# Kernel optimization log

Measured on AMD Instinct MI355X. Metric: run time of the kernel, lower is better.

## Reference

```python
import jax, jax.numpy as jnp
import numpy as np

D_MODEL = 1024
N_HEADS = 16
HEAD_DIM = D_MODEL // N_HEADS


def setup_inputs() -> dict:
    key = jax.random.key(0)
    ks = jax.random.split(key, 9)
    s = 0.02
    x = jax.random.normal(ks[0], (2, 2048, D_MODEL), dtype=jnp.float32)
    wq = jax.random.normal(ks[1], (D_MODEL, D_MODEL), dtype=jnp.float32) * s
    wk = jax.random.normal(ks[2], (D_MODEL, D_MODEL), dtype=jnp.float32) * s
    wv = jax.random.normal(ks[3], (D_MODEL, D_MODEL), dtype=jnp.float32) * s
    wo = jax.random.normal(ks[4], (D_MODEL, D_MODEL), dtype=jnp.float32) * s
    bq = jax.random.normal(ks[5], (D_MODEL,), dtype=jnp.float32) * s
    bk = jax.random.normal(ks[6], (D_MODEL,), dtype=jnp.float32) * s
    bv = jax.random.normal(ks[7], (D_MODEL,), dtype=jnp.float32) * s
    bo = jax.random.normal(ks[8], (D_MODEL,), dtype=jnp.float32) * s
    return {"x": x, "wq": wq, "bq": bq, "wk": wk, "bk": bk,
            "wv": wv, "bv": bv, "wo": wo, "bo": bo}


def reference(x, wq, bq, wk, bk, wv, bv, wo, bo):
    B, T, C = x.shape
    H, Dh = N_HEADS, HEAD_DIM
    # torch Linear: y = x @ W.T + b
    q = (x @ wq.T + bq).reshape(B, T, H, Dh).transpose(0, 2, 1, 3)  # [B,H,T,Dh]
    k = (x @ wk.T + bk).reshape(B, T, H, Dh).transpose(0, 2, 1, 3)
    v = (x @ wv.T + bv).reshape(B, T, H, Dh).transpose(0, 2, 1, 3)
    scale = 1.0 / jnp.sqrt(jnp.float32(Dh))
    score = jnp.einsum('bhqd,bhkd->bhqk', q, k) * scale  # [B,H,T,T]
    causal = jnp.triu(jnp.ones((T, T), dtype=jnp.bool_), k=1)
    score = jnp.where(causal[None, None], jnp.float32(-10000.0), score)
    attn = jax.nn.softmax(score, axis=-1)
    out = jnp.einsum('bhqk,bhkd->bhqd', attn, v)  # [B,H,T,Dh]
    out = out.transpose(0, 2, 1, 3).reshape(B, T, C)
    return out @ wo.T + bo
```

## Files before the change

kernel.cpp:

```cpp
#include <hip/hip_runtime.h>
#include <hip/hip_bf16.h>

typedef __bf16 bf16_t;
typedef __bf16 bf16x8 __attribute__((ext_vector_type(8)));
typedef __bf16 bf16x4 __attribute__((ext_vector_type(4)));
typedef float f32x4 __attribute__((ext_vector_type(4)));
typedef unsigned int u32;

#define D_MODEL 1024
#define T_SEQ   2048
#define N_HEADS 16

#define WAITVM(N) asm volatile("s_waitcnt vmcnt(" #N ")" ::: "memory")

__device__ __forceinline__ void gload_lds16(const void* g, void* l) {
  __builtin_amdgcn_global_load_lds((const __attribute__((address_space(1))) u32*)g,
                                   (__attribute__((address_space(3))) u32*)l, 16, 0, 0);
}

__device__ __forceinline__ float fast_exp2(float x) {
#if __has_builtin(__builtin_amdgcn_exp2f)
  return __builtin_amdgcn_exp2f(x);
#else
  return __expf(x * 0.69314718056f);
#endif
}

struct CastArgs { const float* src[5]; bf16_t* dst[5]; };

__global__ __launch_bounds__(256) void cast_all(CastArgs p) {
  unsigned i = (blockIdx.x * 256u + threadIdx.x) * 4u;
  int seg; unsigned off;
  if (i < 4194304u) { seg = 0; off = i; }
  else { unsigned r = i - 4194304u; seg = 1 + (int)(r >> 20); off = r & 1048575u; }
  const float4 v = *(const float4*)(p.src[seg] + off);
  bf16x4 o = { (bf16_t)v.x, (bf16_t)v.y, (bf16_t)v.z, (bf16_t)v.w };
  *(bf16x4*)(p.dst[seg] + off) = o;
}

#define QSCL 0.18033688011112042f

struct QKVArgs {
  const bf16_t* A;
  const bf16_t* W[3];
  const float* bias[3];
  bf16_t* out[3];
};

__global__ __launch_bounds__(512, 2) void qkv_gemm(QKVArgs p) {
  __shared__ bf16_t lds[2 * 28672];

  const int tid = threadIdx.x;
  const int l = tid & 63, wid = tid >> 6;
  const int lh = l >> 4, r15 = l & 15;

  const int lid = blockIdx.x;
  const int bx = lid >> 4, by = lid & 15;
  const int brow = bx * 256;
  const int gcol0 = by * 192;

  const int wr = (wid >> 2) * 128;
  const int wc = (wid & 3) * 48;
  const int wrc = (wr >> 4);
  const int wcc = (wc >> 4);
  const int sA = (lh ^ ((r15 >> 1) & 3)) * 8;
  const int roff = r15 * 32;

  const int srow = l >> 2;
  const int gs = ((l & 3) ^ ((l >> 3) & 3)) * 8;

  f32x4 acc[8][3];
  const f32x4 zero = {0.f, 0.f, 0.f, 0.f};
#pragma unroll
  for (int i = 0; i < 8; ++i)
#pragma unroll
    for (int j = 0; j < 3; ++j) acc[i][j] = zero;

  const bf16_t* A = p.A;

  auto stageA = [&](bf16_t* buf, int k0, int kh) {
#pragma unroll
    for (int i = 0; i < 2; ++i) {
      int c = wid * 2 + i;
      gload_lds16(A + (size_t)(brow + c * 16 + srow) * D_MODEL + k0 + kh * 32 + gs,
                  buf + kh * 8192 + c * 512);
    }
  };
  auto stageB = [&](bf16_t* buf, int k0) {
#pragma unroll
    for (int i = 0; i < 3; ++i) {
      int g = wid * 3 + i;
      int kh = g >= 12;
      int c = g - kh * 12;
      int gcol = gcol0 + c * 16 + srow;
      int z = gcol >> 10;
      const bf16_t* w = (z == 0) ? p.W[0] : ((z == 1) ? p.W[1] : p.W[2]);
      gload_lds16(w + (size_t)(gcol & 1023) * D_MODEL + k0 + kh * 32 + gs,
                  buf + 16384 + kh * 6144 + c * 512);
    }
  };

  stageA(lds, 0, 0);
  stageA(lds, 0, 1);
  stageB(lds, 0);
  WAITVM(0);
  __builtin_amdgcn_s_barrier();

  for (int t = 0; t < 16; ++t) {
    bf16_t* cur = lds + (t & 1) * 28672;
    bf16_t* nxt = lds + ((t + 1) & 1) * 28672;
    const int k1 = (t + 1) * 64;
    const bool more = (t < 15);

    bf16x8 bfr[3][2];
#pragma unroll
    for (int ph = 0; ph < 4; ++ph) {
      bf16x8 a[2][2];
#pragma unroll
      for (int jj = 0; jj < 2; ++jj)
#pragma unroll
        for (int kh = 0; kh < 2; ++kh)
          a[jj][kh] = *(const bf16x8*)(cur + kh * 8192 + (wrc + 2 * ph + jj) * 512 + roff + sA);
      if (ph == 0) {
#pragma unroll
        for (int ni = 0; ni < 3; ++ni)
#pragma unroll
          for (int kh = 0; kh < 2; ++kh)
            bfr[ni][kh] = *(const bf16x8*)(cur + 16384 + kh * 6144 + (wcc + ni) * 512 + roff + sA);
      }
      if (more) {
        if (ph == 0) stageA(nxt, k1, 0);
        else if (ph == 1) stageA(nxt, k1, 1);
        else if (ph == 2) stageB(nxt, k1);
      }
      __builtin_amdgcn_s_barrier();
      __builtin_amdgcn_s_setprio(1);
#pragma unroll
      for (int jj = 0; jj < 2; ++jj)
#pragma unroll
        for (int ni = 0; ni < 3; ++ni) {
          acc[2 * ph + jj][ni] = __builtin_amdgcn_mfma_f32_16x16x32_bf16(a[jj][0], bfr[ni][0], acc[2 * ph + jj][ni], 0, 0, 0);
          acc[2 * ph + jj][ni] = __builtin_amdgcn_mfma_f32_16x16x32_bf16(a[jj][1], bfr[ni][1], acc[2 * ph + jj][ni], 0, 0, 0);
        }
      __builtin_amdgcn_s_setprio(0);
      if (ph == 3 && more) WAITVM(0);
      __builtin_amdgcn_s_barrier();
    }
  }

#pragma unroll
  for (int ni = 0; ni < 3; ++ni) {
    const int col = gcol0 + wc + ni * 16 + r15;
    const int z = col >> 10;
    const int zc = col & 1023;
    const float* bias = (z == 0) ? p.bias[0] : ((z == 1) ? p.bias[1] : p.bias[2]);
    bf16_t* O = (z == 0) ? p.out[0] : ((z == 1) ? p.out[1] : p.out[2]);
    const float bz = bias[zc];
    if (z == 2) {
#pragma unroll
      for (int mi = 0; mi < 8; ++mi) {
        int row0 = brow + wr + mi * 16 + lh * 4;
        int bb = row0 >> 11, t0 = row0 & 2047;
        bf16x4 pk;
#pragma unroll
        for (int j = 0; j < 4; ++j) pk[j] = (bf16_t)(acc[mi][ni][j] + bz);
        *(bf16x4*)(O + (size_t)bb * (D_MODEL * T_SEQ) + (size_t)zc * T_SEQ + t0) = pk;
      }
    } else if (z == 0) {
#pragma unroll
      for (int mi = 0; mi < 8; ++mi) {
        int row0 = brow + wr + mi * 16 + lh * 4;
#pragma unroll
        for (int j = 0; j < 4; ++j)
          O[(size_t)(row0 + j) * D_MODEL + zc] = (bf16_t)((acc[mi][ni][j] + bz) * QSCL);
      }
    } else {
#pragma unroll
      for (int mi = 0; mi < 8; ++mi) {
        int row0 = brow + wr + mi * 16 + lh * 4;
#pragma unroll
        for (int j = 0; j < 4; ++j)
          O[(size_t)(row0 + j) * D_MODEL + zc] = (bf16_t)(acc[mi][ni][j] + bz);
      }
    }
  }
}

__device__ __forceinline__ void stage_ab64(
    const bf16_t* __restrict__ A, const bf16_t* __restrict__ W,
    bf16_t* buf, int brow, int bcol, int k0, int w, int l) {
  const int srow = l >> 2;
  const int scol = ((l & 3) ^ ((l >> 3) & 3)) * 8;
#pragma unroll
  for (int i = 0; i < 3; ++i) {
    int ch = w * 3 + i;
    const bf16_t* src = (ch < 4)
      ? A + (size_t)(brow + ch * 16 + srow) * D_MODEL + k0 + scol
      : W + (size_t)(bcol + (ch - 4) * 16 + srow) * D_MODEL + k0 + scol;
    gload_lds16(src, buf + ch * 512);
  }
}

__device__ __forceinline__ void gemm_tile_64(
    const bf16_t* __restrict__ A, const bf16_t* __restrict__ W,
    bf16_t* bufs, int brow, int bcol, f32x4 acc[2][4])
{
  const int tid = threadIdx.x;
  const int l = tid & 63, w = tid >> 6;
  const int wr = (w >> 1) * 32, wc = (w & 1) * 64;
  const int lh = l >> 4, r15 = l & 15;
  const int NS = D_MODEL / 32;

  stage_ab64(A, W, bufs + 0 * 6144, brow, bcol, 0, w, l);
  stage_ab64(A, W, bufs + 1 * 6144, brow, bcol, 32, w, l);

  for (int t = 0; t < NS; ++t) {
    bf16_t* bb = bufs + (t % 3) * 6144;
    if (t + 2 < NS) {
      stage_ab64(A, W, bufs + ((t + 2) % 3) * 6144, brow, bcol, (t + 2) * 32, w, l);
      WAITVM(6);
    } else if (t + 1 < NS) {
      WAITVM(3);
    } else {
      WAITVM(0);
    }
    __builtin_amdgcn_s_barrier();

    bf16x8 af[2], bfr[4];
#pragma unroll
    for (int mi = 0; mi < 2; ++mi) {
      int rr = wr + mi * 16 + r15;
      int s = lh ^ ((rr >> 1) & 3);
      af[mi] = *(const bf16x8*)(bb + rr * 32 + s * 8);
    }
#pragma unroll
    for (int ni = 0; ni < 4; ++ni) {
      int rr = wc + ni * 16 + r15;
      int s = lh ^ ((rr >> 1) & 3);
      bfr[ni] = *(const bf16x8*)(bb + 2048 + rr * 32 + s * 8);
    }
    __builtin_amdgcn_s_setprio(1);
#pragma unroll
    for (int mi = 0; mi < 2; ++mi)
#pragma unroll
      for (int ni = 0; ni < 4; ++ni)
        acc[mi][ni] = __builtin_amdgcn_mfma_f32_16x16x32_bf16(af[mi], bfr[ni], acc[mi][ni], 0, 0, 0);
    __builtin_amdgcn_s_setprio(0);
    __builtin_amdgcn_s_barrier();
  }
}

__global__ __launch_bounds__(256) void out_gemm(
    const bf16_t* __restrict__ A, const bf16_t* __restrict__ W,
    const float* __restrict__ bias, float* __restrict__ O)
{
  __shared__ bf16_t bufs[3 * 6144];
  f32x4 acc[2][4];
  f32x4 zero = {0.f, 0.f, 0.f, 0.f};
#pragma unroll
  for (int i = 0; i < 2; ++i)
#pragma unroll
    for (int j = 0; j < 4; ++j) acc[i][j] = zero;

  const int brow = blockIdx.x * 64, bcol = blockIdx.y * 128;
  gemm_tile_64(A, W, bufs, brow, bcol, acc);

  const int tid = threadIdx.x, l = tid & 63, w = tid >> 6;
  const int wr = (w >> 1) * 32, wc = (w & 1) * 64, lh = l >> 4, r15 = l & 15;
#pragma unroll
  for (int ni = 0; ni < 4; ++ni) {
    int col = bcol + wc + ni * 16 + r15;
    float bz = bias[col];
#pragma unroll
    for (int mi = 0; mi < 2; ++mi) {
      int row0 = brow + wr + mi * 16 + lh * 4;
#pragma unroll
      for (int j = 0; j < 4; ++j)
        O[(size_t)(row0 + j) * D_MODEL + col] = acc[mi][ni][j] + bz;
    }
  }
}

__device__ __forceinline__ void stage_kv(const bf16_t* Kg, const bf16_t* Vg,
                                         bf16_t* Kd, bf16_t* Vd, int kv0, int w, int l) {
#pragma unroll
  for (int i = 0; i < 2; ++i) {
    int c = w * 2 + i;
    int rr = c * 8 + (l >> 3);
    int gcol = ((l & 7) ^ ((l >> 3) & 7)) * 8;
    gload_lds16(Kg + (size_t)(kv0 + rr) * D_MODEL + gcol, Kd + c * 512);
    gload_lds16(Vg + (size_t)rr * T_SEQ + kv0 + gcol, Vd + c * 512);
  }
}

__global__ __launch_bounds__(256) void flash_attn(
    const bf16_t* __restrict__ Qm, const bf16_t* __restrict__ Km,
    const bf16_t* __restrict__ Vtg, bf16_t* __restrict__ Om)
{
  __shared__ bf16_t Kls[2][64 * 64];
  __shared__ bf16_t Vls[2][64 * 64];
  __shared__ bf16_t Pls[4][16 * 64];

  const int tid = threadIdx.x, l = tid & 63, w = tid >> 6;
  const int lh = l >> 4, r15 = l & 15;

  const int lid = blockIdx.x;
  const int xcd = lid & 7;
  const int idx = lid >> 3;
  const int pair = idx & 15;
  const int bh = xcd + 8 * (idx >> 4);
  const int b = bh >> 4, h = bh & 15;
  const int qtA = pair, qtB = 31 - pair;

  const size_t baseQ = (size_t)b * T_SEQ * D_MODEL + h * 64;
  const size_t baseVt = (size_t)b * (D_MODEL * T_SEQ) + (size_t)(h * 64) * T_SEQ;
  const bf16_t* Kg = Km + baseQ;
  const bf16_t* Vg = Vtg + baseVt;

  int qw = qtA * 64 + w * 16;

  bf16x8 qf[2];
  {
    const bf16_t* qp = Qm + baseQ + (size_t)(qw + r15) * D_MODEL + lh * 8;
    qf[0] = *(const bf16x8*)(qp);
    qf[1] = *(const bf16x8*)(qp + 32);
  }

  float l_r = 0.f;
  f32x4 o_acc[4];
  const f32x4 zero = {0.f, 0.f, 0.f, 0.f};
#pragma unroll
  for (int n = 0; n < 4; ++n) o_acc[n] = zero;

  bf16_t* P = &Pls[w][0];
  const int NT = 33;

  stage_kv(Kg, Vg, Kls[0], Vls[0], 0, w, l);

  for (int t = 0; t < NT; ++t) {
    const int buf = t & 1;
    if (t + 1 < NT) {
      const int nt = t + 1;
      const int nkv0 = (nt <= qtA) ? nt * 64 : (nt - qtA - 1) * 64;
      stage_kv(Kg, Vg, Kls[buf ^ 1], Vls[buf ^ 1], nkv0, w, l);
      WAITVM(4);
    } else {
      WAITVM(0);
    }
    __builtin_amdgcn_s_barrier();

    const int kv0 = (t <= qtA) ? t * 64 : (t - qtA - 1) * 64;
    const bool diag = (t == qtA) || (t == NT - 1);
    const bf16_t* Kb = Kls[buf];
    const bf16_t* Vb = Vls[buf];

    f32x4 sf[4];
    __builtin_amdgcn_s_setprio(1);
#pragma unroll
    for (int n = 0; n < 4; ++n) {
      const int kvc = n * 16 + r15;
      const int sw = kvc & 7;
      bf16x8 kf0 = *(const bf16x8*)(Kb + kvc * 64 + ((lh ^ sw) * 8));
      bf16x8 kf1 = *(const bf16x8*)(Kb + kvc * 64 + (((4 + lh) ^ sw) * 8));
      f32x4 a = zero;
      a = __builtin_amdgcn_mfma_f32_16x16x32_bf16(kf0, qf[0], a, 0, 0, 0);
      a = __builtin_amdgcn_mfma_f32_16x16x32_bf16(kf1, qf[1], a, 0, 0, 0);
      sf[n] = a;
    }
    __builtin_amdgcn_s_setprio(0);

    const int qrow = qw + r15;
#pragma unroll
    for (int n = 0; n < 4; ++n) {
      float pv[4];
      if (diag) {
#pragma unroll
        for (int j = 0; j < 4; ++j) {
          const int kvcol = kv0 + n * 16 + lh * 4 + j;
          float pp = fast_exp2(sf[n][j]);
          if (kvcol > qrow) pp = 0.f;
          pv[j] = pp;
          l_r += pp;
        }
      } else {
#pragma unroll
        for (int j = 0; j < 4; ++j) {
          float pp = fast_exp2(sf[n][j]);
          pv[j] = pp;
          l_r += pp;
        }
      }
      bf16x4 pk = { (bf16_t)pv[0], (bf16_t)pv[1], (bf16_t)pv[2], (bf16_t)pv[3] };
      const int slot = n * 2 + (lh >> 1);
      *(bf16x4*)(P + r15 * 64 + ((slot ^ (r15 & 7)) * 8) + (lh & 1) * 4) = pk;
    }

    bf16x8 pa0, pa1;
    {
      const int sw = r15 & 7;
      pa0 = *(const bf16x8*)(P + r15 * 64 + ((lh ^ sw) * 8));
      pa1 = *(const bf16x8*)(P + r15 * 64 + (((4 + lh) ^ sw) * 8));
    }
    __builtin_amdgcn_s_setprio(1);
#pragma unroll
    for (int n = 0; n < 4; ++n) {
      const int d = n * 16 + r15;
      const int sw = d & 7;
      bf16x8 vf0 = *(const bf16x8*)(Vb + d * 64 + ((lh ^ sw) * 8));
      bf16x8 vf1 = *(const bf16x8*)(Vb + d * 64 + (((4 + lh) ^ sw) * 8));
      o_acc[n] = __builtin_amdgcn_mfma_f32_16x16x32_bf16(vf0, pa0, o_acc[n], 0, 0, 0);
      o_acc[n] = __builtin_amdgcn_mfma_f32_16x16x32_bf16(vf1, pa1, o_acc[n], 0, 0, 0);
    }
    __builtin_amdgcn_s_setprio(0);

    __builtin_amdgcn_s_barrier();

    if (t == qtA) {
      float ls = l_r;
      ls += __shfl_xor(ls, 16, 64);
      ls += __shfl_xor(ls, 32, 64);
      const float invl = 1.f / ls;
      bf16_t* orow = Om + (size_t)(b * T_SEQ + qw + r15) * D_MODEL + h * 64;
#pragma unroll
      for (int n = 0; n < 4; ++n) {
        bf16x4 pk = { (bf16_t)(o_acc[n][0] * invl), (bf16_t)(o_acc[n][1] * invl),
                      (bf16_t)(o_acc[n][2] * invl), (bf16_t)(o_acc[n][3] * invl) };
        *(bf16x4*)(orow + n * 16 + lh * 4) = pk;
      }
      qw = qtB * 64 + w * 16;
      const bf16_t* qp = Qm + baseQ + (size_t)(qw + r15) * D_MODEL + lh * 8;
      qf[0] = *(const bf16x8*)(qp);
      qf[1] = *(const bf16x8*)(qp + 32);
      l_r = 0.f;
#pragma unroll
      for (int n = 0; n < 4; ++n) o_acc[n] = zero;
    }
  }

  float ls = l_r;
  ls += __shfl_xor(ls, 16, 64);
  ls += __shfl_xor(ls, 32, 64);
  const float invl = 1.f / ls;
  bf16_t* orow = Om + (size_t)(b * T_SEQ + qw + r15) * D_MODEL + h * 64;
#pragma unroll
  for (int n = 0; n < 4; ++n) {
    bf16x4 pk = { (bf16_t)(o_acc[n][0] * invl), (bf16_t)(o_acc[n][1] * invl),
                  (bf16_t)(o_acc[n][2] * invl), (bf16_t)(o_acc[n][3] * invl) };
    *(bf16x4*)(orow + n * 16 + lh * 4) = pk;
  }
}

extern "C" void kernel_launch(void* const* d_in, const int* in_sizes, int n_in,
                              void* d_out, int out_size, void* d_ws, size_t ws_size,
                              hipStream_t stream) {
  const float* x  = (const float*)d_in[0];
  const float* wq = (const float*)d_in[1];
  const float* bq = (const float*)d_in[2];
  const float* wk = (const float*)d_in[3];
  const float* bk = (const float*)d_in[4];
  const float* wv = (const float*)d_in[5];
  const float* bv = (const float*)d_in[6];
  const float* wo = (const float*)d_in[7];
  const float* bo = (const float*)d_in[8];

  char* ws = (char*)d_ws;
  const size_t MB = 1024 * 1024;
  bf16_t* xb  = (bf16_t*)(ws);
  bf16_t* wqb = (bf16_t*)(ws + 8 * MB);
  bf16_t* wkb = (bf16_t*)(ws + 10 * MB);
  bf16_t* wvb = (bf16_t*)(ws + 12 * MB);
  bf16_t* wob = (bf16_t*)(ws + 14 * MB);
  bf16_t* qb  = (bf16_t*)(ws + 16 * MB);
  bf16_t* kb  = (bf16_t*)(ws + 24 * MB);
  bf16_t* vtb = (bf16_t*)(ws + 32 * MB);
  bf16_t* ob  = (bf16_t*)(ws + 40 * MB);

  CastArgs ca;
  ca.src[0] = x;  ca.dst[0] = xb;
  ca.src[1] = wq; ca.dst[1] = wqb;
  ca.src[2] = wk; ca.dst[2] = wkb;
  ca.src[3] = wv; ca.dst[3] = wvb;
  ca.src[4] = wo; ca.dst[4] = wob;
  cast_all<<<8192, 256, 0, stream>>>(ca);

  QKVArgs qa;
  qa.A = xb;
  qa.W[0] = wqb; qa.W[1] = wkb; qa.W[2] = wvb;
  qa.bias[0] = bq; qa.bias[1] = bk; qa.bias[2] = bv;
  qa.out[0] = qb; qa.out[1] = kb; qa.out[2] = vtb;
  qkv_gemm<<<256, 512, 0, stream>>>(qa);

  flash_attn<<<512, 256, 0, stream>>>(qb, kb, vtb, ob);

  out_gemm<<<dim3(64, 8), 256, 0, stream>>>(ob, wob, bo, (float*)d_out);
}
```

Measured before the change: 101.3 us.

## Widen flash-attention KV tiles to 128 and skip masked half on diagonal

Doubles the KV tile staged per iteration from 64 to 128 keys, halving the loop trip count and the number of block barriers per query pair. Softmax and PV are split into two 64-wide halves, and on the diagonal tile the upper half is skipped when the query tile index is even. P staging switches from an XOR swizzle to a padded 72-element row stride, and V uses a 16-way swizzle. LDS use roughly doubles, which may reduce occupancy, and the coarser tiles mean more masked work on odd diagonal tiles.

```diff
diff --git a/kernel.cpp b/kernel.cpp
--- a/kernel.cpp
+++ b/kernel.cpp
@@ -281,15 +281,21 @@
   }
 }
 
-__device__ __forceinline__ void stage_kv(const bf16_t* Kg, const bf16_t* Vg,
-                                         bf16_t* Kd, bf16_t* Vd, int kv0, int w, int l) {
-#pragma unroll
-  for (int i = 0; i < 2; ++i) {
-    int c = w * 2 + i;
-    int rr = c * 8 + (l >> 3);
+__device__ __forceinline__ void stage_kv128(const bf16_t* Kg, const bf16_t* Vg,
+                                            bf16_t* Kd, bf16_t* Vd, int kv0, int w, int l) {
+#pragma unroll
+  for (int i = 0; i < 4; ++i) {
+    int c = w * 4 + i;
+    int row = c * 8 + (l >> 3);
     int gcol = ((l & 7) ^ ((l >> 3) & 7)) * 8;
-    gload_lds16(Kg + (size_t)(kv0 + rr) * D_MODEL + gcol, Kd + c * 512);
-    gload_lds16(Vg + (size_t)rr * T_SEQ + kv0 + gcol, Vd + c * 512);
+    gload_lds16(Kg + (size_t)(kv0 + row) * D_MODEL + gcol, Kd + c * 512);
+  }
+#pragma unroll
+  for (int i = 0; i < 4; ++i) {
+    int c = w * 4 + i;
+    int drow = c * 4 + (l >> 4);
+    int gkv = ((l & 15) ^ (drow & 15)) * 8;
+    gload_lds16(Vg + (size_t)drow * T_SEQ + kv0 + gkv, Vd + c * 512);
   }
 }
 
@@ -297,9 +303,9 @@
     const bf16_t* __restrict__ Qm, const bf16_t* __restrict__ Km,
     const bf16_t* __restrict__ Vtg, bf16_t* __restrict__ Om)
 {
-  __shared__ bf16_t Kls[2][64 * 64];
-  __shared__ bf16_t Vls[2][64 * 64];
-  __shared__ bf16_t Pls[4][16 * 64];
+  __shared__ bf16_t Kls[2][128 * 64];
+  __shared__ bf16_t Vls[2][64 * 128];
+  __shared__ bf16_t Pls[4][16 * 72];
 
   const int tid = threadIdx.x, l = tid & 63, w = tid >> 6;
   const int lh = l >> 4, r15 = l & 15;
@@ -311,6 +317,8 @@
   const int bh = xcd + 8 * (idx >> 4);
   const int b = bh >> 4, h = bh & 15;
   const int qtA = pair, qtB = 31 - pair;
+  const int nA = (qtA >> 1) + 1;
+  const int NT = 17;
 
   const size_t baseQ = (size_t)b * T_SEQ * D_MODEL + h * 64;
   const size_t baseVt = (size_t)b * (D_MODEL * T_SEQ) + (size_t)(h * 64) * T_SEQ;
@@ -333,31 +341,31 @@
   for (int n = 0; n < 4; ++n) o_acc[n] = zero;
 
   bf16_t* P = &Pls[w][0];
-  const int NT = 33;
-
-  stage_kv(Kg, Vg, Kls[0], Vls[0], 0, w, l);
+
+  stage_kv128(Kg, Vg, Kls[0], Vls[0], 0, w, l);
 
   for (int t = 0; t < NT; ++t) {
     const int buf = t & 1;
     if (t + 1 < NT) {
       const int nt = t + 1;
-      const int nkv0 = (nt <= qtA) ? nt * 64 : (nt - qtA - 1) * 64;
-      stage_kv(Kg, Vg, Kls[buf ^ 1], Vls[buf ^ 1], nkv0, w, l);
-      WAITVM(4);
+      const int nkv0 = (nt < nA) ? nt * 128 : (nt - nA) * 128;
+      stage_kv128(Kg, Vg, Kls[buf ^ 1], Vls[buf ^ 1], nkv0, w, l);
+      WAITVM(8);
     } else {
       WAITVM(0);
     }
     __builtin_amdgcn_s_barrier();
 
-    const int kv0 = (t <= qtA) ? t * 64 : (t - qtA - 1) * 64;
-    const bool diag = (t == qtA) || (t == NT - 1);
+    const int kv0 = (t < nA) ? t * 128 : (t - nA) * 128;
+    const int qt_cur = (t < nA) ? qtA : qtB;
+    const bool diag = (t == nA - 1) || (t == NT - 1);
+    const bool skip2 = diag && ((qt_cur & 1) == 0);
     const bf16_t* Kb = Kls[buf];
     const bf16_t* Vb = Vls[buf];
-
-    f32x4 sf[4];
-    __builtin_amdgcn_s_setprio(1);
-#pragma unroll
-    for (int n = 0; n < 4; ++n) {
+    const int qrow = qw + r15;
+
+    f32x4 sf[8];
+    auto qk_n = [&](int n) {
       const int kvc = n * 16 + r15;
       const int sw = kvc & 7;
       bf16x8 kf0 = *(const bf16x8*)(Kb + kvc * 64 + ((lh ^ sw) * 8));
@@ -366,56 +374,68 @@
       a = __builtin_amdgcn_mfma_f32_16x16x32_bf16(kf0, qf[0], a, 0, 0, 0);
       a = __builtin_amdgcn_mfma_f32_16x16x32_bf16(kf1, qf[1], a, 0, 0, 0);
       sf[n] = a;
-    }
-    __builtin_amdgcn_s_setprio(0);
-
-    const int qrow = qw + r15;
-#pragma unroll
-    for (int n = 0; n < 4; ++n) {
-      float pv[4];
-      if (diag) {
+    };
+    auto sm_half = [&](int hh, bool dm) {
+#pragma unroll
+      for (int n2 = 0; n2 < 4; ++n2) {
+        const int n = hh * 4 + n2;
+        float pv[4];
 #pragma unroll
         for (int j = 0; j < 4; ++j) {
-          const int kvcol = kv0 + n * 16 + lh * 4 + j;
           float pp = fast_exp2(sf[n][j]);
-          if (kvcol > qrow) pp = 0.f;
+          if (dm) {
+            const int kvcol = kv0 + hh * 64 + n2 * 16 + lh * 4 + j;
+            if (kvcol > qrow) pp = 0.f;
+          }
           pv[j] = pp;
           l_r += pp;
         }
-      } else {
-#pragma unroll
-        for (int j = 0; j < 4; ++j) {
-          float pp = fast_exp2(sf[n][j]);
-          pv[j] = pp;
-          l_r += pp;
-        }
-      }
-      bf16x4 pk = { (bf16_t)pv[0], (bf16_t)pv[1], (bf16_t)pv[2], (bf16_t)pv[3] };
-      const int slot = n * 2 + (lh >> 1);
-      *(bf16x4*)(P + r15 * 64 + ((slot ^ (r15 & 7)) * 8) + (lh & 1) * 4) = pk;
-    }
-
-    bf16x8 pa0, pa1;
-    {
-      const int sw = r15 & 7;
-      pa0 = *(const bf16x8*)(P + r15 * 64 + ((lh ^ sw) * 8));
-      pa1 = *(const bf16x8*)(P + r15 * 64 + (((4 + lh) ^ sw) * 8));
-    }
+        bf16x4 pk = { (bf16_t)pv[0], (bf16_t)pv[1], (bf16_t)pv[2], (bf16_t)pv[3] };
+        *(bf16x4*)(P + r15 * 72 + (n2 * 2 + (lh >> 1)) * 8 + (lh & 1) * 4) = pk;
+      }
+    };
+    auto pv_half = [&](int hh) {
+      bf16x8 pa0 = *(const bf16x8*)(P + r15 * 72 + lh * 8);
+      bf16x8 pa1 = *(const bf16x8*)(P + r15 * 72 + (4 + lh) * 8);
+      __builtin_amdgcn_s_setprio(1);
+#pragma unroll
+      for (int nD = 0; nD < 4; ++nD) {
+        const int d = nD * 16 + r15;
+        const int b0 = (hh * 8 + lh) ^ r15;
+        const int b1 = (hh * 8 + 4 + lh) ^ r15;
+        bf16x8 vf0 = *(const bf16x8*)(Vb + d * 128 + b0 * 8);
+        bf16x8 vf1 = *(const bf16x8*)(Vb + d * 128 + b1 * 8);
+        o_acc[nD] = __builtin_amdgcn_mfma_f32_16x16x32_bf16(vf0, pa0, o_acc[nD], 0, 0, 0);
+        o_acc[nD] = __builtin_amdgcn_mfma_f32_16x16x32_bf16(vf1, pa1, o_acc[nD], 0, 0, 0);
+      }
+      __builtin_amdgcn_s_setprio(0);
+    };
+
     __builtin_amdgcn_s_setprio(1);
 #pragma unroll
-    for (int n = 0; n < 4; ++n) {
-      const int d = n * 16 + r15;
-      const int sw = d & 7;
-      bf16x8 vf0 = *(const bf16x8*)(Vb + d * 64 + ((lh ^ sw) * 8));
-      bf16x8 vf1 = *(const bf16x8*)(Vb + d * 64 + (((4 + lh) ^ sw) * 8));
-      o_acc[n] = __builtin_amdgcn_mfma_f32_16x16x32_bf16(vf0, pa0, o_acc[n], 0, 0, 0);
-      o_acc[n] = __builtin_amdgcn_mfma_f32_16x16x32_bf16(vf1, pa1, o_acc[n], 0, 0, 0);
-    }
+    for (int n = 0; n < 4; ++n) qk_n(n);
     __builtin_amdgcn_s_setprio(0);
+    if (!skip2) {
+      __builtin_amdgcn_s_setprio(1);
+#pragma unroll
+      for (int n = 4; n < 8; ++n) qk_n(n);
+      __builtin_amdgcn_s_setprio(0);
+    }
+
+    if (diag) {
+      sm_half(0, true);
+      pv_half(0);
+      if (!skip2) { sm_half(1, true); pv_half(1); }
+    } else {
+      sm_half(0, false);
+      pv_half(0);
+      sm_half(1, false);
+      pv_half(1);
+    }
 
     __builtin_amdgcn_s_barrier();
 
-    if (t == qtA) {
+    if (t == nA - 1) {
       float ls = l_r;
       ls += __shfl_xor(ls, 16, 64);
       ls += __shfl_xor(ls, 32, 64);
```

Measured after the change: 97.38 us. 3.9% less time.
